# Performance work log

Measured on AMD Instinct MI355X. Metric: run time of the kernel, lower is better.

The kernel has to match this reference:

```python
import jax, jax.numpy as jnp
import numpy as np

HYP_C = 0.1
TAU = 0.1
MRG = 0.1
CLIP_R = 2.3
BS = 1024
NB_PROXIES = 256
SZ_EMBED = 128
T_BATCH = BS * 50
T_LCA = NB_PROXIES * 50


@jax.custom_vjp
def artanh(x):
    xc = jnp.clip(x, -1.0 + 1e-5, 1.0 - 1e-5)
    return 0.5 * (jnp.log1p(xc) - jnp.log1p(-xc))

def _artanh_fwd(x):
    xc = jnp.clip(x, -1.0 + 1e-5, 1.0 - 1e-5)
    return 0.5 * (jnp.log1p(xc) - jnp.log1p(-xc)), xc

def _artanh_bwd(xc, g):
    return (g / (1.0 - xc * xc),)

artanh.defvjp(_artanh_fwd, _artanh_bwd)


@jax.custom_vjp
def riemannian_fix(x):
    # identity fwd; bwd rescales euclidean grad to riemannian grad on the ball
    return x

def _riem_fwd(x):
    return x, x

def _riem_bwd(x, g):
    scale = ((1.0 - HYP_C * jnp.sum(x * x, axis=-1, keepdims=True)) ** 2) / 4.0
    return (g * scale,)

riemannian_fix.defvjp(_riem_fwd, _riem_bwd)


def expmap0(x, c):
    sqrt_c = c ** 0.5
    xn = jnp.maximum(jnp.linalg.norm(x, axis=-1, keepdims=True), 1e-5)
    return jnp.tanh(sqrt_c * xn) * x / (sqrt_c * xn)


def project(x, c):
    norm = jnp.maximum(jnp.linalg.norm(x, axis=-1, keepdims=True), 1e-5)
    maxnorm = (1.0 - 1e-3) / (c ** 0.5)
    return jnp.where(norm > maxnorm, x / norm * maxnorm, x)


def to_poincare(x, c, clip_r):
    xn = jnp.linalg.norm(x, axis=-1, keepdims=True) + 1e-5
    x = x * jnp.minimum(jnp.ones_like(xn), clip_r / xn)
    return riemannian_fix(project(expmap0(x, c), c))


def dist_matrix(x, y, c):
    # ||mobius_add(-x, y)|| computed in closed form (same math as the [N,M,D]
    # num/denom construction in the torch code; num_{nm} = a*( -x_n ) + b*y_m).
    sqrt_c = c ** 0.5
    xy = -jnp.einsum('nd,md->nm', x, y)        # (-x) . y
    x2 = jnp.sum(x * x, axis=-1, keepdims=True)  # [N,1]
    y2t = jnp.sum(y * y, axis=-1)[None, :]       # [1,M]
    a = 1.0 + 2.0 * c * xy + c * y2t             # coeff of -x
    b = 1.0 - c * x2                             # coeff of y
    denom = 1.0 + 2.0 * c * xy + (c ** 2) * x2 * y2t
    num_sq = a * a * x2 + 2.0 * a * b * xy + b * b * y2t
    norm = jnp.sqrt(jnp.maximum(num_sq, 1e-12)) / jnp.abs(denom + 1e-5)
    return (2.0 / sqrt_c) * artanh(sqrt_c * norm)


def gumbel_softmax_hard(logits, g):
    # straight-through hard gumbel softmax (tau=1 as in F.gumbel_softmax default)
    y = jax.nn.softmax(logits + g, axis=-1)
    hard = jax.nn.one_hot(jnp.argmax(y, axis=-1), y.shape[-1], dtype=y.dtype)
    return y + jax.lax.stop_gradient(hard - y)


def compute_ghhc(cp_dist, trip, g):
    i, j, k = trip[0], trip[1], trip[2]
    di, dj, dk = cp_dist[i], cp_dist[j], cp_dist[k]   # [T,P] each
    max_ij = jnp.maximum(di, dj)
    p_ij = gumbel_softmax_hard(-max_ij / TAU, g[0])
    max_ijk = jnp.maximum(dk, max_ij)
    p_ijk = gumbel_softmax_hard(-max_ijk / TAU, g[1])
    diff_lca = (jnp.argmax(p_ij, -1) != jnp.argmax(p_ijk, -1)).astype(cp_dist.dtype)
    d_i_ij = jnp.sum(di * p_ij, axis=1)
    d_i_ijk = jnp.sum(di * p_ijk, axis=1)
    d_j_ij = jnp.sum(dj * p_ij, axis=1)
    d_j_ijk = jnp.sum(dj * p_ijk, axis=1)
    d_k_ij = jnp.sum(dk * p_ij, axis=1)
    d_k_ijk = jnp.sum(dk * p_ijk, axis=1)
    hc = (jax.nn.relu(d_i_ij - d_i_ijk + MRG)
          + jax.nn.relu(d_j_ij - d_j_ijk + MRG)
          + jax.nn.relu(d_k_ijk - d_k_ij + MRG))
    return jnp.mean(hc * diff_lca)


def hp_loss(z_s, t_s, lcas, trip1, trip2, trip3, trip4, g1, g2, g3, g4):
    bs = z_s.shape[0]
    lh = to_poincare(lcas, HYP_C, CLIP_R)
    all_nodes = jnp.concatenate([z_s, lh], axis=0)
    D = dist_matrix(all_nodes, all_nodes, HYP_C)
    t_all = jnp.concatenate([t_s, lh], axis=0)
    Dt = dist_matrix(t_all, t_all, HYP_C)
    loss = compute_ghhc(D[:bs, bs:], trip1, g1)
    loss = loss + compute_ghhc(D[bs:, bs:], trip2, g2)
    loss = loss + compute_ghhc(Dt[:bs, bs:], trip3, g3)
    loss = loss + compute_ghhc(Dt[bs:, bs:], trip4, g4)
    return loss


def setup_inputs() -> dict:
    key = jax.random.key(0)
    ks = jax.random.split(key, 12)
    z_s = jax.random.normal(ks[0], (BS, SZ_EMBED), dtype=jnp.float32)
    t_s = jax.random.normal(ks[1], (BS, SZ_EMBED), dtype=jnp.float32)
    y = jax.random.uniform(ks[2], (BS, 24), dtype=jnp.float32)
    # lcas param init: randn / sqrt(d) * clip_r * 0.9
    lcas = jax.random.normal(ks[3], (NB_PROXIES, SZ_EMBED), dtype=jnp.float32)
    lcas = lcas / np.sqrt(SZ_EMBED) * CLIP_R * 0.9
    trip1 = jax.random.randint(ks[4], (3, T_BATCH), 0, BS, dtype=jnp.int32)
    trip2 = jax.random.randint(ks[5], (3, T_LCA), 0, NB_PROXIES, dtype=jnp.int32)
    trip3 = jax.random.randint(ks[6], (3, T_BATCH), 0, BS, dtype=jnp.int32)
    trip4 = jax.random.randint(ks[7], (3, T_LCA), 0, NB_PROXIES, dtype=jnp.int32)
    g1 = jax.random.gumbel(ks[8], (2, T_BATCH, NB_PROXIES), dtype=jnp.float32)
    g2 = jax.random.gumbel(ks[9], (2, T_LCA, NB_PROXIES), dtype=jnp.float32)
    g3 = jax.random.gumbel(ks[10], (2, T_BATCH, NB_PROXIES), dtype=jnp.float32)
    g4 = jax.random.gumbel(ks[11], (2, T_LCA, NB_PROXIES), dtype=jnp.float32)
    return {"z_s": z_s, "t_s": t_s, "y": y, "lcas": lcas,
            "trip1": trip1, "trip2": trip2, "trip3": trip3, "trip4": trip4,
            "g1": g1, "g2": g2, "g3": g3, "g4": g4}


def reference(z_s, t_s, y, lcas, trip1, trip2, trip3, trip4, g1, g2, g3, g4):
    # y only feeds the detached numpy mining loop in the original; the mined
    # triplets are supplied precomputed (trip1..4), so y does not enter the math.
    return hp_loss(z_s, t_s, lcas, trip1, trip2, trip3, trip4, g1, g2, g3, g4)
```

## Files before the change

### kernel.cpp

```cpp
#include <hip/hip_runtime.h>
#include <cstddef>
#include <stdint.h>

#define HYP_C   0.1f
#define SQRT_C  0.31622776601683794f
#define CLIP_R  2.3f
#define MRG     0.1f
#define NPROX   256
#define DIM     128

#define OFF_LH   0
#define OFF_LHT  32768
#define OFF_LN2  65536
#define OFF_D1   65792
#define OFF_D2   327936
#define OFF_D3   393472

__global__ __launch_bounds__(128)
void to_poincare_kernel(const float* __restrict__ lcas,
                        float* __restrict__ ws,
                        float* __restrict__ out)
{
    const int row = blockIdx.x;
    const int k   = threadIdx.x;
    if (row == 0 && k == 0) out[0] = 0.0f;

    float v  = lcas[row * DIM + k];
    float ss = v * v;
    #pragma unroll
    for (int off = 32; off >= 1; off >>= 1)
        ss += __shfl_xor(ss, off, 64);
    __shared__ float wpart[2];
    if ((k & 63) == 0) wpart[k >> 6] = ss;
    __syncthreads();
    const float sumsq = wpart[0] + wpart[1];

    const float s1 = sqrtf(sumsq);
    const float xn = s1 + 1e-5f;
    const float f1 = fminf(1.0f, CLIP_R / xn);
    const float xn2 = fmaxf(f1 * s1, 1e-5f);
    const float th  = tanhf(SQRT_C * xn2);
    const float f2  = th / (SQRT_C * xn2);
    const float nr      = fmaxf(f2 * f1 * s1, 1e-5f);
    const float maxnorm = (1.0f - 1e-3f) / SQRT_C;
    const float f3      = (nr > maxnorm) ? (maxnorm / nr) : 1.0f;

    const float f  = f3 * f2 * f1;
    const float lv = f * v;
    ws[OFF_LH  + row * DIM + k]   = lv;
    ws[OFF_LHT + k * NPROX + row] = lv;
    if (k == 0) ws[OFF_LN2 + row] = f * f * sumsq;
}

__global__ __launch_bounds__(256)
void dist_all_kernel(const float* __restrict__ z,
                     const float* __restrict__ t,
                     float* __restrict__ ws, int nb1)
{
    const float* lhT = ws + OFF_LHT;
    const float* ln2 = ws + OFF_LN2;

    int b = blockIdx.x;
    const float* X; float* Dout; int row0;
    if (b < nb1)            { X = z;            Dout = ws + OFF_D1; row0 = b * 4; }
    else if (b < nb1 + 64)  { X = ws + OFF_LH;  Dout = ws + OFF_D2; row0 = (b - nb1) * 4; }
    else                    { X = t;            Dout = ws + OFF_D3; row0 = (b - nb1 - 64) * 4; }

    __shared__ float xs[4][DIM];
    __shared__ float sx2[4];

    for (int idx = threadIdx.x; idx < 4 * DIM; idx += 256)
        xs[idx / DIM][idx % DIM] = X[row0 * DIM + idx];
    __syncthreads();

    const int wid  = threadIdx.x >> 6;
    const int lane = threadIdx.x & 63;
    {
        float a = xs[wid][lane];
        float c = xs[wid][lane + 64];
        float s = a * a + c * c;
        #pragma unroll
        for (int off = 32; off >= 1; off >>= 1)
            s += __shfl_xor(s, off, 64);
        if (lane == 0) sx2[wid] = s;
    }
    __syncthreads();

    const int m = threadIdx.x;
    float dot0 = 0.f, dot1 = 0.f, dot2 = 0.f, dot3 = 0.f;
    #pragma unroll 8
    for (int k = 0; k < DIM; k += 4) {
        const float4 x0 = *(const float4*)&xs[0][k];
        const float4 x1 = *(const float4*)&xs[1][k];
        const float4 x2 = *(const float4*)&xs[2][k];
        const float4 x3 = *(const float4*)&xs[3][k];
        const float l0 = lhT[(k + 0) * NPROX + m];
        const float l1 = lhT[(k + 1) * NPROX + m];
        const float l2 = lhT[(k + 2) * NPROX + m];
        const float l3 = lhT[(k + 3) * NPROX + m];
        dot0 = fmaf(x0.x, l0, fmaf(x0.y, l1, fmaf(x0.z, l2, fmaf(x0.w, l3, dot0))));
        dot1 = fmaf(x1.x, l0, fmaf(x1.y, l1, fmaf(x1.z, l2, fmaf(x1.w, l3, dot1))));
        dot2 = fmaf(x2.x, l0, fmaf(x2.y, l1, fmaf(x2.z, l2, fmaf(x2.w, l3, dot2))));
        dot3 = fmaf(x3.x, l0, fmaf(x3.y, l1, fmaf(x3.z, l2, fmaf(x3.w, l3, dot3))));
    }

    const float y2 = ln2[m];
    float dots[4] = {dot0, dot1, dot2, dot3};
    #pragma unroll
    for (int r = 0; r < 4; ++r) {
        const float x2 = sx2[r];
        const float xy = -dots[r];
        const float a  = 1.0f + 2.0f * HYP_C * xy + HYP_C * y2;
        const float bb = 1.0f - HYP_C * x2;
        const float denom  = 1.0f + 2.0f * HYP_C * xy + HYP_C * HYP_C * x2 * y2;
        const float num_sq = a * a * x2 + 2.0f * a * bb * xy + bb * bb * y2;
        const float nrm = sqrtf(fmaxf(num_sq, 1e-12f)) / fabsf(denom + 1e-5f);
        float u = SQRT_C * nrm;
        u = fminf(fmaxf(u, -1.0f + 1e-5f), 1.0f - 1e-5f);
        const float d = (2.0f / SQRT_C) * (0.5f * (log1pf(u) - log1pf(-u)));
        Dout[(size_t)(row0 + r) * NPROX + m] = d;
    }
}

__device__ __forceinline__ float dpp_fmax16(float x) {
    int o;
    o = __builtin_amdgcn_update_dpp(0, __float_as_int(x), 0x121, 0xF, 0xF, true);
    x = fmaxf(x, __int_as_float(o));
    o = __builtin_amdgcn_update_dpp(0, __float_as_int(x), 0x122, 0xF, 0xF, true);
    x = fmaxf(x, __int_as_float(o));
    o = __builtin_amdgcn_update_dpp(0, __float_as_int(x), 0x124, 0xF, 0xF, true);
    x = fmaxf(x, __int_as_float(o));
    o = __builtin_amdgcn_update_dpp(0, __float_as_int(x), 0x128, 0xF, 0xF, true);
    x = fmaxf(x, __int_as_float(o));
    return x;
}

__device__ __forceinline__ int dpp_imin16(int x) {
    int o;
    o = __builtin_amdgcn_update_dpp(0, x, 0x121, 0xF, 0xF, true); x = min(x, o);
    o = __builtin_amdgcn_update_dpp(0, x, 0x122, 0xF, 0xF, true); x = min(x, o);
    o = __builtin_amdgcn_update_dpp(0, x, 0x124, 0xF, 0xF, true); x = min(x, o);
    o = __builtin_amdgcn_update_dpp(0, x, 0x128, 0xF, 0xF, true); x = min(x, o);
    return x;
}

__global__ __launch_bounds__(256, 3)
void ghhc_fused_kernel(const float* __restrict__ Da, const float* __restrict__ Db,
                       const float* __restrict__ Dc, const float* __restrict__ Dd,
                       const int* __restrict__ ta, const int* __restrict__ tb,
                       const int* __restrict__ tc, const int* __restrict__ td,
                       const float* __restrict__ ga, const float* __restrict__ gb,
                       const float* __restrict__ gc, const float* __restrict__ gd,
                       int Ta, int Tb, int Tc, int Td,
                       float sa, float sb, float sc_, float sd,
                       int nba, int nbb, int nbc,
                       float* __restrict__ out)
{
    const int tid = threadIdx.x;
    const int w   = tid >> 6;
    const int grp = (tid >> 4) & 3;
    const int hl  = tid & 15;
    const int hl4 = hl << 2;

    const int b = blockIdx.x;
    const float* D; const int* tr; const float* g; int Tt; float sc; int lb;
    if (b < nba)                   { D = Da; tr = ta; g = ga; Tt = Ta; sc = sa;  lb = b; }
    else if (b < nba + nbb)        { D = Db; tr = tb; g = gb; Tt = Tb; sc = sb;  lb = b - nba; }
    else if (b < nba + nbb + nbc)  { D = Dc; tr = tc; g = gc; Tt = Tc; sc = sc_; lb = b - nba - nbb; }
    else                           { D = Dd; tr = td; g = gd; Tt = Td; sc = sd;  lb = b - nba - nbb - nbc; }

    const int tstart = lb * 64 + w * 16;

    int iIt[4], jIt[4], kIt[4], tIt[4]; bool okIt[4];
    #pragma unroll
    for (int it = 0; it < 4; ++it) {
        int t = tstart + it * 4 + grp;
        okIt[it] = (t < Tt);
        t = okIt[it] ? t : (Tt - 1);
        tIt[it] = t;
        iIt[it] = tr[t]; jIt[it] = tr[Tt + t]; kIt[it] = tr[2 * Tt + t];
    }

    float dif[16], djf[16], dkf[16], g0f[16], g1f[16];

    #define ISSUE(IT) { \
        const float4* Di_ = (const float4*)(D + (size_t)iIt[IT] * NPROX); \
        const float4* Dj_ = (const float4*)(D + (size_t)jIt[IT] * NPROX); \
        const float4* Dk_ = (const float4*)(D + (size_t)kIt[IT] * NPROX); \
        const float4* G0_ = (const float4*)(g + (size_t)tIt[IT] * NPROX); \
        const float4* G1_ = (const float4*)(g + ((size_t)Tt + tIt[IT]) * NPROX); \
        _Pragma("unroll") \
        for (int m_ = 0; m_ < 4; ++m_) { \
            const int q_ = m_ * 16 + hl; \
            float4 v_; \
            v_ = Di_[q_]; dif[m_*4+0]=v_.x; dif[m_*4+1]=v_.y; dif[m_*4+2]=v_.z; dif[m_*4+3]=v_.w; \
            v_ = Dj_[q_]; djf[m_*4+0]=v_.x; djf[m_*4+1]=v_.y; djf[m_*4+2]=v_.z; djf[m_*4+3]=v_.w; \
            v_ = Dk_[q_]; dkf[m_*4+0]=v_.x; dkf[m_*4+1]=v_.y; dkf[m_*4+2]=v_.z; dkf[m_*4+3]=v_.w; \
            v_ = G0_[q_]; g0f[m_*4+0]=v_.x; g0f[m_*4+1]=v_.y; g0f[m_*4+2]=v_.z; g0f[m_*4+3]=v_.w; \
            v_ = G1_[q_]; g1f[m_*4+0]=v_.x; g1f[m_*4+1]=v_.y; g1f[m_*4+2]=v_.z; g1f[m_*4+3]=v_.w; \
        } }

    float acc = 0.0f;
    float pdiA = 0.f, pdjA = 0.f, pdkA = 0.f, pdiB = 0.f, pdjB = 0.f, pdkB = 0.f;
    bool  pC = false;

    ISSUE(0);

    #pragma unroll
    for (int it = 0; it < 4; ++it) {
        float Sf[16], Uf[16];
        #pragma unroll
        for (int c = 0; c < 16; ++c) {
            const float m1 = fmaxf(dif[c], djf[c]);
            Sf[c] = fmaf(m1, -10.0f, g0f[c]);
            const float m2 = fmaxf(dkf[c], m1);
            Uf[c] = fmaf(m2, -10.0f, g1f[c]);
        }

        if (it == 0)      ISSUE(1)
        else if (it == 1) ISSUE(2)
        else if (it == 2) ISSUE(3)

        float lvA = Sf[0], lvB = Uf[0];
        #pragma unroll
        for (int c = 1; c < 16; ++c) { lvA = fmaxf(lvA, Sf[c]); lvB = fmaxf(lvB, Uf[c]); }
        const float gvA = dpp_fmax16(lvA);
        const float gvB = dpp_fmax16(lvB);

        int slA = 64, slB = 64;
        #pragma unroll
        for (int c = 15; c >= 0; --c) {
            slA = (Sf[c] == gvA) ? c : slA;
            slB = (Uf[c] == gvB) ? c : slB;
        }
        const int eA = (slA < 16) ? (((slA & 12) << 4) | (hl4 | (slA & 3))) : 1024;
        const int eB = (slB < 16) ? (((slB & 12) << 4) | (hl4 | (slB & 3))) : 1024;
        const int Ag = dpp_imin16(eA);
        const int Bg = dpp_imin16(eB);

        const float* Ri = D + (size_t)iIt[it] * NPROX;
        const float* Rj = D + (size_t)jIt[it] * NPROX;
        const float* Rk = D + (size_t)kIt[it] * NPROX;
        const float eDiA = Ri[Ag], eDiB = Ri[Bg];
        const float eDjA = Rj[Ag], eDjB = Rj[Bg];
        const float eDkA = Rk[Ag], eDkB = Rk[Bg];

        if (it > 0) {
            const float hc = fmaxf(pdiA - pdiB + MRG, 0.0f)
                           + fmaxf(pdjA - pdjB + MRG, 0.0f)
                           + fmaxf(pdkB - pdkA + MRG, 0.0f);
            acc += (pC && (hl == 0)) ? hc * sc : 0.0f;
        }

        pdiA = eDiA; pdiB = eDiB;
        pdjA = eDjA; pdjB = eDjB;
        pdkA = eDkA; pdkB = eDkB;
        pC = okIt[it] && (Ag != Bg);
    }
    #undef ISSUE

    {
        const float hc = fmaxf(pdiA - pdiB + MRG, 0.0f)
                       + fmaxf(pdjA - pdjB + MRG, 0.0f)
                       + fmaxf(pdkB - pdkA + MRG, 0.0f);
        acc += (pC && (hl == 0)) ? hc * sc : 0.0f;
    }

    acc += __shfl_xor(acc, 16, 64);
    acc += __shfl_xor(acc, 32, 64);
    __shared__ float wsum[4];
    if ((tid & 63) == 0) wsum[w] = acc;
    __syncthreads();
    if (tid == 0)
        atomicAdd(out, wsum[0] + wsum[1] + wsum[2] + wsum[3]);
}

extern "C" void kernel_launch(void* const* d_in, const int* in_sizes, int n_in,
                              void* d_out, int out_size, void* d_ws, size_t ws_size,
                              hipStream_t stream)
{
    const float* z_s  = (const float*)d_in[0];
    const float* t_s  = (const float*)d_in[1];
    const float* lcas = (const float*)d_in[3];
    const int* trip1 = (const int*)d_in[4];
    const int* trip2 = (const int*)d_in[5];
    const int* trip3 = (const int*)d_in[6];
    const int* trip4 = (const int*)d_in[7];
    const float* g1 = (const float*)d_in[8];
    const float* g2 = (const float*)d_in[9];
    const float* g3 = (const float*)d_in[10];
    const float* g4 = (const float*)d_in[11];
    float* out = (float*)d_out;
    float* ws  = (float*)d_ws;

    const int T1 = in_sizes[4] / 3;
    const int T2 = in_sizes[5] / 3;
    const int T3 = in_sizes[6] / 3;
    const int T4 = in_sizes[7] / 3;
    const int BS = in_sizes[0] / DIM;
    const int nb1 = BS / 4;

    to_poincare_kernel<<<NPROX, 128, 0, stream>>>(lcas, ws, out);

    dist_all_kernel<<<2 * nb1 + 64, 256, 0, stream>>>(z_s, t_s, ws, nb1);

    const int nbA = (T1 + 63) / 64;
    const int nbB = (T2 + 63) / 64;
    const int nbC = (T3 + 63) / 64;
    const int nbD = (T4 + 63) / 64;
    ghhc_fused_kernel<<<nbA + nbB + nbC + nbD, 256, 0, stream>>>(
        ws + OFF_D1, ws + OFF_D2, ws + OFF_D3, ws + OFF_D2,
        trip1, trip2, trip3, trip4,
        g1, g2, g3, g4,
        T1, T2, T3, T4,
        1.0f / (float)T1, 1.0f / (float)T2, 1.0f / (float)T3, 1.0f / (float)T4,
        nbA, nbB, nbC,
        out);
}
```

Baseline: 298.7 us.

## Process one triplet per wave with 3-deep load pipeline instead of 16-lane groups

Restructures the gumbel-argmax kernel so each 64-lane wave handles one triplet at a time, with each lane holding a single float4 of every row, rather than four triplets per wave spread across 16-lane groups of 16 floats each. Row loads are issued three triplets ahead through a rotating register buffer, and triplet indices are broadcast with shuffles. Reductions now span the whole wave using DPP plus cross-row shuffles, and the occupancy hint rises from 3 to 4 blocks per CU. The intent is lower register pressure and deeper memory-level parallelism, at the cost of more cross-lane reduction steps per triplet.

```diff
diff --git a/kernel.cpp b/kernel.cpp
--- a/kernel.cpp
+++ b/kernel.cpp
@@ -144,7 +144,21 @@
     return x;
 }
 
-__global__ __launch_bounds__(256, 3)
+__device__ __forceinline__ float wave_fmax(float x) {
+    x = dpp_fmax16(x);
+    x = fmaxf(x, __shfl_xor(x, 16, 64));
+    x = fmaxf(x, __shfl_xor(x, 32, 64));
+    return x;
+}
+
+__device__ __forceinline__ int wave_imin(int x) {
+    x = dpp_imin16(x);
+    x = min(x, __shfl_xor(x, 16, 64));
+    x = min(x, __shfl_xor(x, 32, 64));
+    return x;
+}
+
+__global__ __launch_bounds__(256, 4)
 void ghhc_fused_kernel(const float* __restrict__ Da, const float* __restrict__ Db,
                        const float* __restrict__ Dc, const float* __restrict__ Dd,
                        const int* __restrict__ ta, const int* __restrict__ tb,
@@ -156,11 +170,9 @@
                        int nba, int nbb, int nbc,
                        float* __restrict__ out)
 {
-    const int tid = threadIdx.x;
-    const int w   = tid >> 6;
-    const int grp = (tid >> 4) & 3;
-    const int hl  = tid & 15;
-    const int hl4 = hl << 2;
+    const int tid  = threadIdx.x;
+    const int w    = tid >> 6;
+    const int lane = tid & 63;
 
     const int b = blockIdx.x;
     const float* D; const int* tr; const float* g; int Tt; float sc; int lb;
@@ -171,105 +183,93 @@
 
     const int tstart = lb * 64 + w * 16;
 
-    int iIt[4], jIt[4], kIt[4], tIt[4]; bool okIt[4];
-    #pragma unroll
-    for (int it = 0; it < 4; ++it) {
-        int t = tstart + it * 4 + grp;
-        okIt[it] = (t < Tt);
-        t = okIt[it] ? t : (Tt - 1);
-        tIt[it] = t;
-        iIt[it] = tr[t]; jIt[it] = tr[Tt + t]; kIt[it] = tr[2 * Tt + t];
-    }
-
-    float dif[16], djf[16], dkf[16], g0f[16], g1f[16];
+    int tl = tstart + (lane & 15);
+    tl = (tl < Tt) ? tl : (Tt - 1);
+    const int idxi = tr[tl];
+    const int idxj = tr[Tt + tl];
+    const int idxk = tr[2 * Tt + tl];
+
+    float4 bdi[3], bdj[3], bdk[3], bg0[3], bg1[3];
 
     #define ISSUE(IT) { \
-        const float4* Di_ = (const float4*)(D + (size_t)iIt[IT] * NPROX); \
-        const float4* Dj_ = (const float4*)(D + (size_t)jIt[IT] * NPROX); \
-        const float4* Dk_ = (const float4*)(D + (size_t)kIt[IT] * NPROX); \
-        const float4* G0_ = (const float4*)(g + (size_t)tIt[IT] * NPROX); \
-        const float4* G1_ = (const float4*)(g + ((size_t)Tt + tIt[IT]) * NPROX); \
-        _Pragma("unroll") \
-        for (int m_ = 0; m_ < 4; ++m_) { \
-            const int q_ = m_ * 16 + hl; \
-            float4 v_; \
-            v_ = Di_[q_]; dif[m_*4+0]=v_.x; dif[m_*4+1]=v_.y; dif[m_*4+2]=v_.z; dif[m_*4+3]=v_.w; \
-            v_ = Dj_[q_]; djf[m_*4+0]=v_.x; djf[m_*4+1]=v_.y; djf[m_*4+2]=v_.z; djf[m_*4+3]=v_.w; \
-            v_ = Dk_[q_]; dkf[m_*4+0]=v_.x; dkf[m_*4+1]=v_.y; dkf[m_*4+2]=v_.z; dkf[m_*4+3]=v_.w; \
-            v_ = G0_[q_]; g0f[m_*4+0]=v_.x; g0f[m_*4+1]=v_.y; g0f[m_*4+2]=v_.z; g0f[m_*4+3]=v_.w; \
-            v_ = G1_[q_]; g1f[m_*4+0]=v_.x; g1f[m_*4+1]=v_.y; g1f[m_*4+2]=v_.z; g1f[m_*4+3]=v_.w; \
-        } }
+        const int t_  = tstart + (IT); \
+        const int te_ = (t_ < Tt) ? t_ : (Tt - 1); \
+        const int i_  = __shfl(idxi, (IT) & 15, 64); \
+        const int j_  = __shfl(idxj, (IT) & 15, 64); \
+        const int k_  = __shfl(idxk, (IT) & 15, 64); \
+        bdi[(IT) % 3] = ((const float4*)(D + (size_t)i_ * NPROX))[lane]; \
+        bdj[(IT) % 3] = ((const float4*)(D + (size_t)j_ * NPROX))[lane]; \
+        bdk[(IT) % 3] = ((const float4*)(D + (size_t)k_ * NPROX))[lane]; \
+        bg0[(IT) % 3] = ((const float4*)(g + (size_t)te_ * NPROX))[lane]; \
+        bg1[(IT) % 3] = ((const float4*)(g + ((size_t)Tt + te_) * NPROX))[lane]; \
+    }
 
     float acc = 0.0f;
     float pdiA = 0.f, pdjA = 0.f, pdkA = 0.f, pdiB = 0.f, pdjB = 0.f, pdkB = 0.f;
     bool  pC = false;
 
-    ISSUE(0);
-
-    #pragma unroll
-    for (int it = 0; it < 4; ++it) {
-        float Sf[16], Uf[16];
-        #pragma unroll
-        for (int c = 0; c < 16; ++c) {
-            const float m1 = fmaxf(dif[c], djf[c]);
-            Sf[c] = fmaf(m1, -10.0f, g0f[c]);
-            const float m2 = fmaxf(dkf[c], m1);
-            Uf[c] = fmaf(m2, -10.0f, g1f[c]);
-        }
-
-        if (it == 0)      ISSUE(1)
-        else if (it == 1) ISSUE(2)
-        else if (it == 2) ISSUE(3)
-
-        float lvA = Sf[0], lvB = Uf[0];
-        #pragma unroll
-        for (int c = 1; c < 16; ++c) { lvA = fmaxf(lvA, Sf[c]); lvB = fmaxf(lvB, Uf[c]); }
-        const float gvA = dpp_fmax16(lvA);
-        const float gvB = dpp_fmax16(lvB);
-
-        int slA = 64, slB = 64;
-        #pragma unroll
-        for (int c = 15; c >= 0; --c) {
-            slA = (Sf[c] == gvA) ? c : slA;
-            slB = (Uf[c] == gvB) ? c : slB;
-        }
-        const int eA = (slA < 16) ? (((slA & 12) << 4) | (hl4 | (slA & 3))) : 1024;
-        const int eB = (slB < 16) ? (((slB & 12) << 4) | (hl4 | (slB & 3))) : 1024;
-        const int Ag = dpp_imin16(eA);
-        const int Bg = dpp_imin16(eB);
-
-        const float* Ri = D + (size_t)iIt[it] * NPROX;
-        const float* Rj = D + (size_t)jIt[it] * NPROX;
-        const float* Rk = D + (size_t)kIt[it] * NPROX;
-        const float eDiA = Ri[Ag], eDiB = Ri[Bg];
-        const float eDjA = Rj[Ag], eDjB = Rj[Bg];
-        const float eDkA = Rk[Ag], eDkB = Rk[Bg];
-
-        if (it > 0) {
-            const float hc = fmaxf(pdiA - pdiB + MRG, 0.0f)
-                           + fmaxf(pdjA - pdjB + MRG, 0.0f)
-                           + fmaxf(pdkB - pdkA + MRG, 0.0f);
-            acc += (pC && (hl == 0)) ? hc * sc : 0.0f;
-        }
-
-        pdiA = eDiA; pdiB = eDiB;
-        pdjA = eDjA; pdjB = eDjB;
-        pdkA = eDkA; pdkB = eDkB;
-        pC = okIt[it] && (Ag != Bg);
-    }
+    ISSUE(0); ISSUE(1); ISSUE(2);
+
+    #define STEP(IT) { \
+        const float4 di = bdi[(IT) % 3]; \
+        const float4 dj = bdj[(IT) % 3]; \
+        const float4 dk = bdk[(IT) % 3]; \
+        const float4 q0 = bg0[(IT) % 3]; \
+        const float4 q1 = bg1[(IT) % 3]; \
+        float S0, S1, S2, S3, U0, U1, U2, U3; \
+        { float m1, m2; \
+          m1 = fmaxf(di.x, dj.x); S0 = fmaf(m1, -10.0f, q0.x); m2 = fmaxf(dk.x, m1); U0 = fmaf(m2, -10.0f, q1.x); \
+          m1 = fmaxf(di.y, dj.y); S1 = fmaf(m1, -10.0f, q0.y); m2 = fmaxf(dk.y, m1); U1 = fmaf(m2, -10.0f, q1.y); \
+          m1 = fmaxf(di.z, dj.z); S2 = fmaf(m1, -10.0f, q0.z); m2 = fmaxf(dk.z, m1); U2 = fmaf(m2, -10.0f, q1.z); \
+          m1 = fmaxf(di.w, dj.w); S3 = fmaf(m1, -10.0f, q0.w); m2 = fmaxf(dk.w, m1); U3 = fmaf(m2, -10.0f, q1.w); } \
+        if ((IT) + 3 < 16) ISSUE((IT) + 3) \
+        const float gvA = wave_fmax(fmaxf(fmaxf(S0, S1), fmaxf(S2, S3))); \
+        const float gvB = wave_fmax(fmaxf(fmaxf(U0, U1), fmaxf(U2, U3))); \
+        int slA = 4, slB = 4; \
+        slA = (S3 == gvA) ? 3 : slA; slA = (S2 == gvA) ? 2 : slA; \
+        slA = (S1 == gvA) ? 1 : slA; slA = (S0 == gvA) ? 0 : slA; \
+        slB = (U3 == gvB) ? 3 : slB; slB = (U2 == gvB) ? 2 : slB; \
+        slB = (U1 == gvB) ? 1 : slB; slB = (U0 == gvB) ? 0 : slB; \
+        const int eA = (slA < 4) ? ((lane << 2) | slA) : 1024; \
+        const int eB = (slB < 4) ? ((lane << 2) | slB) : 1024; \
+        const int Ag = wave_imin(eA); \
+        const int Bg = wave_imin(eB); \
+        const int i_ = __shfl(idxi, (IT) & 15, 64); \
+        const int j_ = __shfl(idxj, (IT) & 15, 64); \
+        const int k_ = __shfl(idxk, (IT) & 15, 64); \
+        const float* Ri = D + (size_t)i_ * NPROX; \
+        const float* Rj = D + (size_t)j_ * NPROX; \
+        const float* Rk = D + (size_t)k_ * NPROX; \
+        const float nDiA = Ri[Ag], nDiB = Ri[Bg]; \
+        const float nDjA = Rj[Ag], nDjB = Rj[Bg]; \
+        const float nDkA = Rk[Ag], nDkB = Rk[Bg]; \
+        if ((IT) > 0) { \
+            const float hc = fmaxf(pdiA - pdiB + MRG, 0.0f) \
+                           + fmaxf(pdjA - pdjB + MRG, 0.0f) \
+                           + fmaxf(pdkB - pdkA + MRG, 0.0f); \
+            acc += (pC && lane == 0) ? hc * sc : 0.0f; \
+        } \
+        pdiA = nDiA; pdiB = nDiB; pdjA = nDjA; pdjB = nDjB; pdkA = nDkA; pdkB = nDkB; \
+        pC = ((tstart + (IT)) < Tt) && (Ag != Bg); \
+    }
+
+    STEP(0)  STEP(1)  STEP(2)  STEP(3)
+    STEP(4)  STEP(5)  STEP(6)  STEP(7)
+    STEP(8)  STEP(9)  STEP(10) STEP(11)
+    STEP(12) STEP(13) STEP(14) STEP(15)
+
+    #undef STEP
     #undef ISSUE
 
     {
         const float hc = fmaxf(pdiA - pdiB + MRG, 0.0f)
                        + fmaxf(pdjA - pdjB + MRG, 0.0f)
                        + fmaxf(pdkB - pdkA + MRG, 0.0f);
-        acc += (pC && (hl == 0)) ? hc * sc : 0.0f;
-    }
-
-    acc += __shfl_xor(acc, 16, 64);
-    acc += __shfl_xor(acc, 32, 64);
+        acc += (pC && lane == 0) ? hc * sc : 0.0f;
+    }
+
     __shared__ float wsum[4];
-    if ((tid & 63) == 0) wsum[w] = acc;
+    if (lane == 0) wsum[w] = acc;
     __syncthreads();
     if (tid == 0)
         atomicAdd(out, wsum[0] + wsum[1] + wsum[2] + wsum[3]);
```

After: 379.5 us. 1.27x slower.
